# Kernel tuning notes

Measured on AMD Instinct MI355X. Metric: run time of the kernel, lower is better.

## Reference

```python
import jax, jax.numpy as jnp
import numpy as np

# LeNet-5 custom connectivity between S2 (6 ch) and C3 (16 ch): MAP[i, o] = 1 if input ch i feeds output ch o
MAP_INFO = np.array([
    [1, 0, 0, 0, 1, 1, 1, 0, 0, 1, 1, 1, 1, 0, 1, 1],
    [1, 1, 0, 0, 0, 1, 1, 1, 0, 0, 1, 1, 1, 1, 0, 1],
    [1, 1, 1, 0, 0, 0, 1, 1, 1, 0, 0, 1, 0, 1, 1, 1],
    [0, 1, 1, 1, 0, 0, 1, 1, 1, 1, 0, 0, 1, 0, 1, 1],
    [0, 0, 1, 1, 1, 0, 0, 1, 1, 1, 1, 0, 1, 1, 0, 1],
    [0, 0, 0, 1, 1, 1, 0, 0, 1, 1, 1, 1, 0, 1, 1, 1],
], dtype=np.float32)  # [6, 16]

SCALE = 1.7159
SLOPE = 2.0 / 3.0


def _conv(x, w):
    # x: [B, Cin, H, W], w: [Cout, Cin, kh, kw], VALID padding, stride 1
    return jax.lax.conv_general_dilated(
        x, w, window_strides=(1, 1), padding='VALID',
        dimension_numbers=('NCHW', 'OIHW', 'NCHW'))


def _subsample(x, w, b):
    # 2x2 average pool then per-channel affine (trainable scale/bias)
    B, C, H, W = x.shape
    p = x.reshape(B, C, H // 2, 2, W // 2, 2).mean(axis=(3, 5))
    return p * w[None, :, None, None] + b[None, :, None, None]


def _act(x):
    return SCALE * jnp.tanh(SLOPE * x)


def setup_inputs() -> dict:
    key = jax.random.key(0)
    ks = jax.random.split(key, 16)
    B = 8192

    def unif(k, shape, fan_in):
        return (jax.random.uniform(k, shape, dtype=jnp.float32) * 4.8 - 2.4) / fan_in

    x = jax.random.normal(ks[0], (B, 1, 32, 32), dtype=jnp.float32)
    c1_w = unif(ks[1], (6, 1, 5, 5), 25 * 1)
    c1_b = jax.random.uniform(ks[2], (6,), dtype=jnp.float32) * 0.1
    s2_w = unif(ks[3], (6,), 4)
    s2_b = jax.random.uniform(ks[4], (6,), dtype=jnp.float32)
    c3_w = unif(ks[5], (16, 6, 5, 5), 25 * 6)
    c3_b = jax.random.uniform(ks[6], (16,), dtype=jnp.float32) * 0.1
    s4_w = unif(ks[7], (16,), 4)
    s4_b = jax.random.uniform(ks[8], (16,), dtype=jnp.float32)
    c5_w = unif(ks[9], (120, 16, 5, 5), 25 * 16)
    c5_b = jax.random.uniform(ks[10], (120,), dtype=jnp.float32) * 0.1
    f6_w = unif(ks[11], (84, 120), 120)
    f6_b = jax.random.uniform(ks[12], (84,), dtype=jnp.float32) * 0.1
    rbf_w = jax.random.uniform(ks[13], (84, 10), dtype=jnp.float32)
    return dict(x=x, c1_w=c1_w, c1_b=c1_b, s2_w=s2_w, s2_b=s2_b,
                c3_w=c3_w, c3_b=c3_b, s4_w=s4_w, s4_b=s4_b,
                c5_w=c5_w, c5_b=c5_b, f6_w=f6_w, f6_b=f6_b, rbf_w=rbf_w)


def reference(x, c1_w, c1_b, s2_w, s2_b, c3_w, c3_b, s4_w, s4_b,
              c5_w, c5_b, f6_w, f6_b, rbf_w):
    # C1: 1->6 conv5, replicate padding 2 -> [B,6,32,32]
    xp = jnp.pad(x, ((0, 0), (0, 0), (2, 2), (2, 2)), mode='edge')
    h = _conv(xp, c1_w) + c1_b[None, :, None, None]
    # S2 + squashing act -> [B,6,16,16]
    h = _act(_subsample(h, s2_w, s2_b))
    # C3: sparse-connectivity conv expressed as dense conv with masked weights -> [B,16,12,12]
    mask = jnp.asarray(MAP_INFO.T)[:, :, None, None]  # [16,6,1,1]
    h = _conv(h, c3_w * mask) + c3_b[None, :, None, None]
    # S4 + act -> [B,16,6,6]
    h = _act(_subsample(h, s4_w, s4_b))
    # C5: 16->120 conv5 -> [B,120,1,1]
    h = _conv(h, c5_w) + c5_b[None, :, None, None]
    h = h.reshape(-1, 120)
    # F6 + act -> [B,84]
    h = _act(h @ f6_w.T + f6_b)
    # RBF output: squared euclidean distance to class prototypes -> [B,10]
    out = jnp.sum((h[:, :, None] - rbf_w[None, :, :]) ** 2, axis=1)
    return out
```

## Files before the change

kernel.cpp:

```cpp
#include <hip/hip_runtime.h>
#include <math.h>

typedef _Float16 h16;
typedef h16  h8v __attribute__((ext_vector_type(8)));
typedef h16  h4v __attribute__((ext_vector_type(4)));
typedef h16  h2v __attribute__((ext_vector_type(2)));
typedef float f4v __attribute__((ext_vector_type(4)));
typedef unsigned int u32;
typedef u32  u4v __attribute__((ext_vector_type(4)));
typedef u32  u2v __attribute__((ext_vector_type(2)));

#if defined(__has_builtin)
#if __has_builtin(__builtin_amdgcn_fdot2)
#define FDOT2(a,b,c) __builtin_amdgcn_fdot2((a),(b),(c),false)
#endif
#endif
#ifndef FDOT2
#define FDOT2(a,b,c) ((c) + (float)(a).x*(float)(b).x + (float)(a).y*(float)(b).y)
#endif

#define WS_K1H  0
#define WS_B1   216
#define WS_B3   224
#define WS_W3H  240
#define WS_W5H  2544
#define WS_F6H  35312
#define WS_RBFT 41456

#define L_B3    0
#define L_C5B   64
#define L_F6B   576
#define L_S2H   960
#define L_S4    960
#define L_HB    960
#define L_A6    6592
#define L_XPADH 14784
#define L_AI    14784
#define L_A5    14784
#define LDS_TOTAL 31424

__device__ const unsigned char MASK16[16] = {7,14,28,56,49,35,15,30,60,57,51,39,27,54,45,63};

__device__ __forceinline__ float squash(float x) {
    float z = (2.0f / 3.0f) * x;
    float a = fabsf(z);
    float e = __expf(-2.0f * a);
    float t = (1.0f - e) * __builtin_amdgcn_rcpf(1.0f + e);
    return copysignf(1.7159f * t, z);
}

__global__ __launch_bounds__(256) void prep_kernel(
    const float* __restrict__ c1_w, const float* __restrict__ c1_b,
    const float* __restrict__ s2_w, const float* __restrict__ s2_b,
    const float* __restrict__ c3_w, const float* __restrict__ c3_b,
    const float* __restrict__ s4_w, const float* __restrict__ s4_b,
    const float* __restrict__ c5_w, const float* __restrict__ f6_w,
    const float* __restrict__ rbf_w,
    float* __restrict__ ws)
{
    const int gid = blockIdx.x * 256 + threadIdx.x;
    const int gstr = gridDim.x * 256;
    h16* K1H = (h16*)ws;
    for (int idx = gid; idx < 216; idx += gstr) {
        int c = idx / 36, r = idx - c * 36;
        int u = r / 6, v = r - u * 6;
        float s = 0.f;
        #pragma unroll
        for (int dy = 0; dy < 2; ++dy)
            #pragma unroll
            for (int dx = 0; dx < 2; ++dx) {
                int ky = u - dy, kx = v - dx;
                if (ky >= 0 && ky < 5 && kx >= 0 && kx < 5)
                    s += c1_w[(c * 5 + ky) * 5 + kx];
            }
        K1H[idx] = (h16)(0.25f * s * s2_w[c]);
    }
    if (gid < 6)  ws[WS_B1 + gid] = s2_w[gid] * c1_b[gid] + s2_b[gid];
    if (gid < 16) ws[WS_B3 + gid] = s4_w[gid] * c3_b[gid] + s4_b[gid];
    h16* W3H = (h16*)(ws + WS_W3H);
    for (int idx = gid; idx < 4608; idx += gstr) {
        int i = idx / 768, r = idx - i * 768;
        int n = r / 48, k = r - n * 48;
        float val = 0.f;
        if (k < 36) {
            int u = k / 6, v = k - u * 6;
            float s = 0.f;
            #pragma unroll
            for (int dy = 0; dy < 2; ++dy)
                #pragma unroll
                for (int dx = 0; dx < 2; ++dx) {
                    int ky = u - dy, kx = v - dx;
                    if (ky >= 0 && ky < 5 && kx >= 0 && kx < 5)
                        s += c3_w[((n * 6 + i) * 5 + ky) * 5 + kx];
                }
            val = ((MASK16[n] >> i) & 1) ? 0.25f * s4_w[n] * s : 0.f;
        }
        W3H[idx] = (h16)val;
    }
    h16* W5H = (h16*)(ws + WS_W5H);
    for (int idx = gid; idx < 65536; idx += gstr) {
        int i = idx >> 12, r = idx & 4095;
        int n = r >> 5, k = r & 31;
        float val = (n < 120 && k < 25) ? c5_w[n * 400 + i * 25 + k] : 0.f;
        W5H[idx] = (h16)val;
    }
    h16* F6H = (h16*)(ws + WS_F6H);
    for (int idx = gid; idx < 12288; idx += gstr) {
        int n = idx >> 7, k = idx & 127;
        float val = (n < 84 && k < 120) ? f6_w[n * 120 + k] : 0.f;
        F6H[idx] = (h16)val;
    }
    for (int idx = gid; idx < 840; idx += gstr) {
        int k = idx / 10, c = idx - k * 10;
        ws[WS_RBFT + c * 84 + k] = rbf_w[idx];
    }
}

__global__ __launch_bounds__(256, 5) void lenet_kernel(
    const float* __restrict__ x,
    const float* __restrict__ c5_b, const float* __restrict__ f6_b,
    const float* __restrict__ ws,
    float* __restrict__ out)
{
    __shared__ __align__(16) char smem[LDS_TOTAL];
    float* s_b3  = (float*)(smem + L_B3);
    float* s_c5b = (float*)(smem + L_C5B);
    float* s_f6b = (float*)(smem + L_F6B);
    h16*  XPADH  = (h16*)(smem + L_XPADH);
    h16*  S2H    = (h16*)(smem + L_S2H);
    h16*  AI     = (h16*)(smem + L_AI);
    h16*  S4     = (h16*)(smem + L_S4);
    h16*  A5     = (h16*)(smem + L_A5);
    h16*  A6     = (h16*)(smem + L_A6);
    float* HB    = (float*)(smem + L_HB);

    const int tid  = threadIdx.x;
    const int wave = __builtin_amdgcn_readfirstlane(tid >> 6);
    const int lane = tid & 63;
    const int quad = lane >> 4;
    const int lr   = lane & 15;

    if (tid < 16)  s_b3[tid] = ws[WS_B3 + tid];
    if (tid < 128) s_c5b[tid] = (tid < 120) ? c5_b[tid] : 0.f;
    if (tid < 96)  s_f6b[tid] = (tid < 84) ? f6_b[tid] : 0.f;
    const float* xb = x + (size_t)blockIdx.x * 4096;
    for (int idx = tid; idx < 2880; idx += 256) {
        int img = idx / 720, r2 = idx - img * 720;
        int u = r2 / 20, v2 = r2 - u * 20;
        int sy = min(max(u - 2, 0), 31);
        int c0 = min(max(2 * v2 - 2, 0), 31);
        int c1 = min(max(2 * v2 - 1, 0), 31);
        const float* xr = xb + img * 1024 + sy * 32;
        h2v hv; hv.x = (h16)xr[c0]; hv.y = (h16)xr[c1];
        *(h2v*)(XPADH + img * 1440 + u * 40 + 2 * v2) = hv;
    }
    __syncthreads();

    {
        int py = tid >> 4, px = tid & 15;
        h2v win2[4][18];
        #pragma unroll
        for (int img = 0; img < 4; ++img) {
            const h16* basep = XPADH + img * 1440 + (2 * py) * 40 + 2 * px;
            #pragma unroll
            for (int u = 0; u < 6; ++u)
                #pragma unroll
                for (int p = 0; p < 3; ++p)
                    win2[img][u * 3 + p] = *(const h2v*)(basep + u * 40 + 2 * p);
        }
        const h2v* K1H = (const h2v*)ws;
        #pragma unroll
        for (int c = 0; c < 6; ++c) {
            float bias = ws[WS_B1 + c];
            h2v wv[18];
            #pragma unroll
            for (int j = 0; j < 18; ++j) wv[j] = K1H[c * 18 + j];
            #pragma unroll
            for (int img = 0; img < 4; ++img) {
                float acc = bias;
                #pragma unroll
                for (int j = 0; j < 18; ++j)
                    acc = FDOT2(win2[img][j], wv[j], acc);
                S2H[img * 1728 + c * 288 + py * 18 + px] = (h16)squash(acc);
            }
        }
    }
    __syncthreads();

    {
        const h16* W3H = (const h16*)(ws + WS_W3H);
        h8v w3a[6]; h4v w3b[6];
        #pragma unroll
        for (int i = 0; i < 6; ++i) {
            const h16* bbase = W3H + i * 768 + lr * 48;
            w3a[i] = *(const h8v*)(bbase + quad * 8);
            w3b[i] = *(const h4v*)(bbase + 32 + quad * 4);
        }
        for (int t = tid; t < 1440; t += 256) {
            int row = t / 10, j = t - row * 10;
            *(u32*)(AI + row * 56 + 36 + 2 * j) = 0u;
        }
        const int rowv = (tid < 144) ? tid : 0;
        const int imgR = rowv / 36, posR = rowv - imgR * 36;
        const int pyR = posR / 6, pxR = posR - pyR * 6;
        const h16* srcR = S2H + imgR * 1728 + (2 * pyR) * 18 + 2 * pxR;
        h16* dstR = AI + rowv * 56;
        f4v cacc[3] = {};
        for (int i = 0; i < 6; ++i) {
            if (tid < 144) {
                const h16* src = srcR + i * 288;
                u32 wrow[18];
                #pragma unroll
                for (int u = 0; u < 6; ++u) {
                    wrow[u*3+0] = *(const u32*)(src + u * 18);
                    wrow[u*3+1] = *(const u32*)(src + u * 18 + 2);
                    wrow[u*3+2] = *(const u32*)(src + u * 18 + 4);
                }
                *(u4v*)(dstR)      = (u4v){wrow[0],  wrow[1],  wrow[2],  wrow[3]};
                *(u4v*)(dstR + 8)  = (u4v){wrow[4],  wrow[5],  wrow[6],  wrow[7]};
                *(u4v*)(dstR + 16) = (u4v){wrow[8],  wrow[9],  wrow[10], wrow[11]};
                *(u4v*)(dstR + 24) = (u4v){wrow[12], wrow[13], wrow[14], wrow[15]};
                *(u2v*)(dstR + 32) = (u2v){wrow[16], wrow[17]};
            }
            __syncthreads();
            #pragma unroll
            for (int s = 0; s < 3; ++s) {
                int Mt = wave + 4 * s;
                if (Mt < 9) {
                    const h16* ar = AI + (Mt * 16 + lr) * 56;
                    h8v a8 = *(const h8v*)(ar + quad * 8);
                    cacc[s] = __builtin_amdgcn_mfma_f32_16x16x32_f16(a8, w3a[i], cacc[s], 0, 0, 0);
                    h4v a4 = *(const h4v*)(ar + 32 + quad * 4);
                    cacc[s] = __builtin_amdgcn_mfma_f32_16x16x16f16(a4, w3b[i], cacc[s], 0, 0, 0);
                }
            }
            if (i < 5) __syncthreads();
        }
        #pragma unroll
        for (int s = 0; s < 3; ++s) {
            int Mt = wave + 4 * s;
            if (Mt < 9) {
                #pragma unroll
                for (int r = 0; r < 4; ++r) {
                    int m = Mt * 16 + quad * 4 + r;
                    int img = m / 36, pos = m - img * 36;
                    float v = cacc[s][r] + s_b3[lr];
                    S4[img * 672 + lr * 42 + pos] = (h16)squash(v);
                }
            }
        }
    }
    __syncthreads();

    {
        {
            int m = tid >> 4, i = tid & 15;
            int img = m >> 2, q = m & 3, qy = q >> 1, qx = q & 1;
            const h16* s4b = S4 + img * 672 + i * 42 + qy * 6 + qx;
            h16* dst = A5 + m * 520 + i * 32;
            #pragma unroll
            for (int c = 0; c < 4; ++c) {
                h8v v;
                #pragma unroll
                for (int j = 0; j < 8; ++j) {
                    int k = c * 8 + j;
                    v[j] = (k < 25) ? s4b[(k / 5) * 6 + (k % 5)] : (h16)0.f;
                }
                *(h8v*)(dst + c * 8) = v;
            }
        }
        __syncthreads();
        const h16* W5H = (const h16*)(ws + WS_W5H);
        f4v dacc[2] = {};
        #pragma unroll 4
        for (int i = 0; i < 16; ++i) {
            h8v bf0 = *(const h8v*)(W5H + i * 4096 + (wave * 32 + lr) * 32 + quad * 8);
            h8v bf1 = *(const h8v*)(W5H + i * 4096 + (wave * 32 + 16 + lr) * 32 + quad * 8);
            h8v af0 = *(const h8v*)(A5 + lr * 520 + i * 32 + quad * 8);
            dacc[0] = __builtin_amdgcn_mfma_f32_16x16x32_f16(af0, bf0, dacc[0], 0, 0, 0);
            dacc[1] = __builtin_amdgcn_mfma_f32_16x16x32_f16(af0, bf1, dacc[1], 0, 0, 0);
        }
        if (tid < 64) {
            int m = tid >> 2, j = tid & 3;
            *(u32*)(A6 + m * 136 + 120 + 2 * j) = 0u;
        }
        #pragma unroll
        for (int nt = 0; nt < 2; ++nt) {
            int n = wave * 32 + nt * 16 + lr;
            if (n < 120) {
                int tt = n / 30, cb = (n - tt * 30) * 4;
                float bias = s_c5b[n];
                #pragma unroll
                for (int r = 0; r < 4; ++r) {
                    int m = quad * 4 + r;
                    int img = m >> 2, q = m & 3;
                    A6[(img * 4 + tt) * 136 + cb + q] = (h16)(dacc[nt][r] + bias);
                }
            }
        }
    }
    __syncthreads();

    {
        const h16* F6H = (const h16*)(ws + WS_F6H);
        f4v eacc[2] = {};
        #pragma unroll
        for (int kc = 0; kc < 4; ++kc) {
            h8v a8 = *(const h8v*)(A6 + lr * 136 + kc * 32 + quad * 8);
            h8v b0 = *(const h8v*)(F6H + (wave * 16 + lr) * 128 + kc * 32 + quad * 8);
            eacc[0] = __builtin_amdgcn_mfma_f32_16x16x32_f16(a8, b0, eacc[0], 0, 0, 0);
            if (wave < 2) {
                h8v b1 = *(const h8v*)(F6H + ((wave + 4) * 16 + lr) * 128 + kc * 32 + quad * 8);
                eacc[1] = __builtin_amdgcn_mfma_f32_16x16x32_f16(a8, b1, eacc[1], 0, 0, 0);
            }
        }
        {
            int n = wave * 16 + lr;
            float bias = s_f6b[n];
            #pragma unroll
            for (int r = 0; r < 4; ++r) {
                int m = quad * 4 + r;
                HB[m * 88 + n] = squash(eacc[0][r] + bias);
            }
        }
        if (wave < 2) {
            int n = (wave + 4) * 16 + lr;
            if (n < 84) {
                float bias = s_f6b[n];
                #pragma unroll
                for (int r = 0; r < 4; ++r) {
                    int m = quad * 4 + r;
                    HB[m * 88 + n] = squash(eacc[1][r] + bias);
                }
            }
        }
    }
    __syncthreads();

    if (tid < 160) {
        int m = tid / 10, cls = tid - m * 10;
        const float4* hr = (const float4*)(HB + m * 88);
        const float4* pr = (const float4*)(ws + WS_RBFT + cls * 84);
        float a = 0.f;
        #pragma unroll
        for (int u = 0; u < 21; ++u) {
            float4 hv = hr[u], pv = pr[u];
            float dx = hv.x - pv.x, dy = hv.y - pv.y;
            float dz = hv.z - pv.z, dw = hv.w - pv.w;
            a += dx * dx + dy * dy + dz * dz + dw * dw;
        }
        out[(size_t)blockIdx.x * 160 + tid] = a;
    }
}

extern "C" void kernel_launch(void* const* d_in, const int* in_sizes, int n_in,
                              void* d_out, int out_size, void* d_ws, size_t ws_size,
                              hipStream_t stream) {
    (void)n_in; (void)out_size; (void)ws_size;
    const float* x     = (const float*)d_in[0];
    const float* c1_w  = (const float*)d_in[1];
    const float* c1_b  = (const float*)d_in[2];
    const float* s2_w  = (const float*)d_in[3];
    const float* s2_b  = (const float*)d_in[4];
    const float* c3_w  = (const float*)d_in[5];
    const float* c3_b  = (const float*)d_in[6];
    const float* s4_w  = (const float*)d_in[7];
    const float* s4_b  = (const float*)d_in[8];
    const float* c5_w  = (const float*)d_in[9];
    const float* c5_b  = (const float*)d_in[10];
    const float* f6_w  = (const float*)d_in[11];
    const float* f6_b  = (const float*)d_in[12];
    const float* rbf_w = (const float*)d_in[13];
    float* out = (float*)d_out;
    float* ws  = (float*)d_ws;

    const int B = in_sizes[0] / 1024;

    prep_kernel<<<256, 256, 0, stream>>>(c1_w, c1_b, s2_w, s2_b, c3_w, c3_b,
                                         s4_w, s4_b, c5_w, f6_w, rbf_w, ws);
    lenet_kernel<<<B / 4, 256, 0, stream>>>(x, c5_b, f6_b, ws, out);
}
```

Baseline: 149.4 us.

## Gather C3 MFMA operands directly from S2 LDS, dropping im2col staging buffer

```diff
diff --git a/kernel.cpp b/kernel.cpp
--- a/kernel.cpp
+++ b/kernel.cpp
@@ -7,8 +7,6 @@
 typedef h16  h2v __attribute__((ext_vector_type(2)));
 typedef float f4v __attribute__((ext_vector_type(4)));
 typedef unsigned int u32;
-typedef u32  u4v __attribute__((ext_vector_type(4)));
-typedef u32  u2v __attribute__((ext_vector_type(2)));
 
 #if defined(__has_builtin)
 #if __has_builtin(__builtin_amdgcn_fdot2)
@@ -31,13 +29,12 @@
 #define L_C5B   64
 #define L_F6B   576
 #define L_S2H   960
-#define L_S4    960
+#define L_A5    960
 #define L_HB    960
-#define L_A6    6592
 #define L_XPADH 14784
-#define L_AI    14784
-#define L_A5    14784
-#define LDS_TOTAL 31424
+#define L_S4    20160
+#define L_A6    20160
+#define LDS_TOTAL 26304
 
 __device__ const unsigned char MASK16[16] = {7,14,28,56,49,35,15,30,60,57,51,39,27,54,45,63};
 
@@ -116,7 +113,7 @@
     }
 }
 
-__global__ __launch_bounds__(256, 5) void lenet_kernel(
+__global__ __launch_bounds__(256, 6) void lenet_kernel(
     const float* __restrict__ x,
     const float* __restrict__ c5_b, const float* __restrict__ f6_b,
     const float* __restrict__ ws,
@@ -128,7 +125,6 @@
     float* s_f6b = (float*)(smem + L_F6B);
     h16*  XPADH  = (h16*)(smem + L_XPADH);
     h16*  S2H    = (h16*)(smem + L_S2H);
-    h16*  AI     = (h16*)(smem + L_AI);
     h16*  S4     = (h16*)(smem + L_S4);
     h16*  A5     = (h16*)(smem + L_A5);
     h16*  A6     = (h16*)(smem + L_A6);
@@ -196,45 +192,39 @@
             w3a[i] = *(const h8v*)(bbase + quad * 8);
             w3b[i] = *(const h4v*)(bbase + 32 + quad * 4);
         }
-        for (int t = tid; t < 1440; t += 256) {
-            int row = t / 10, j = t - row * 10;
-            *(u32*)(AI + row * 56 + 36 + 2 * j) = 0u;
-        }
-        const int rowv = (tid < 144) ? tid : 0;
-        const int imgR = rowv / 36, posR = rowv - imgR * 36;
-        const int pyR = posR / 6, pxR = posR - pyR * 6;
-        const h16* srcR = S2H + imgR * 1728 + (2 * pyR) * 18 + 2 * pxR;
-        h16* dstR = AI + rowv * 56;
+        const int OQA[4] = {0, 20, 40, 72};
+        const int OQB[4] = {2, 22, 54, 74};
+        const int OQC[4] = {4, 36, 56, 76};
+        const int OQD[4] = {18, 38, 58, 90};
+        const int o0 = OQA[quad], o1 = OQB[quad], o2 = OQC[quad], o3 = OQD[quad];
+        int baseh[3];
+        #pragma unroll
+        for (int s = 0; s < 3; ++s) {
+            int Mt = wave + 4 * s;
+            int m = Mt * 16 + lr; if (m > 143) m = 143;
+            int img = m / 36, pos = m - img * 36;
+            int py = pos / 6, px = pos - py * 6;
+            baseh[s] = img * 1728 + (2 * py) * 18 + 2 * px;
+        }
         f4v cacc[3] = {};
         for (int i = 0; i < 6; ++i) {
-            if (tid < 144) {
-                const h16* src = srcR + i * 288;
-                u32 wrow[18];
-                #pragma unroll
-                for (int u = 0; u < 6; ++u) {
-                    wrow[u*3+0] = *(const u32*)(src + u * 18);
-                    wrow[u*3+1] = *(const u32*)(src + u * 18 + 2);
-                    wrow[u*3+2] = *(const u32*)(src + u * 18 + 4);
-                }
-                *(u4v*)(dstR)      = (u4v){wrow[0],  wrow[1],  wrow[2],  wrow[3]};
-                *(u4v*)(dstR + 8)  = (u4v){wrow[4],  wrow[5],  wrow[6],  wrow[7]};
-                *(u4v*)(dstR + 16) = (u4v){wrow[8],  wrow[9],  wrow[10], wrow[11]};
-                *(u4v*)(dstR + 24) = (u4v){wrow[12], wrow[13], wrow[14], wrow[15]};
-                *(u2v*)(dstR + 32) = (u2v){wrow[16], wrow[17]};
-            }
-            __syncthreads();
             #pragma unroll
             for (int s = 0; s < 3; ++s) {
                 int Mt = wave + 4 * s;
                 if (Mt < 9) {
-                    const h16* ar = AI + (Mt * 16 + lr) * 56;
-                    h8v a8 = *(const h8v*)(ar + quad * 8);
-                    cacc[s] = __builtin_amdgcn_mfma_f32_16x16x32_f16(a8, w3a[i], cacc[s], 0, 0, 0);
-                    h4v a4 = *(const h4v*)(ar + 32 + quad * 4);
-                    cacc[s] = __builtin_amdgcn_mfma_f32_16x16x16f16(a4, w3b[i], cacc[s], 0, 0, 0);
-                }
-            }
-            if (i < 5) __syncthreads();
+                    const h16* bp = S2H + baseh[s] + i * 288;
+                    union { u32 u[4]; h8v h; } av;
+                    av.u[0] = *(const u32*)(bp + o0);
+                    av.u[1] = *(const u32*)(bp + o1);
+                    av.u[2] = *(const u32*)(bp + o2);
+                    av.u[3] = *(const u32*)(bp + o3);
+                    cacc[s] = __builtin_amdgcn_mfma_f32_16x16x32_f16(av.h, w3a[i], cacc[s], 0, 0, 0);
+                    union { u32 u[2]; h4v h; } av2;
+                    av2.u[0] = *(const u32*)(bp + 92);
+                    av2.u[1] = *(const u32*)(bp + 94);
+                    cacc[s] = __builtin_amdgcn_mfma_f32_16x16x16f16(av2.h, w3b[i], cacc[s], 0, 0, 0);
+                }
+            }
         }
         #pragma unroll
         for (int s = 0; s < 3; ++s) {
```

New measurement: 154.7 us. +3.6%, slower.
